# Kernel tuning notes

Hardware: AMD Instinct MI355X
Metric: run time of the kernel (lower is better)

The kernel has to match this reference:

```python
import jax, jax.numpy as jnp
import numpy as np

EMBED_DIM = 1024
NUM_HEAD = 16
HEAD_DIM = EMBED_DIM // NUM_HEAD
SCALE = HEAD_DIM ** -0.5
EPS = 1e-6


def setup_inputs() -> dict:
    key = jax.random.key(0)
    ks = jax.random.split(key, 8)
    B, N, K, D = 4, 2048, 2048, EMBED_DIM
    x = jax.random.normal(ks[0], (B, N, D), dtype=jnp.float32)
    ctx = jax.random.normal(ks[1], (B, K, D), dtype=jnp.float32)
    w_std = 0.02
    q_w = jax.random.normal(ks[2], (D, D), dtype=jnp.float32) * w_std  # [in, out]
    q_b = jnp.zeros((D,), dtype=jnp.float32)
    kv_w = jax.random.normal(ks[3], (D, 2 * D), dtype=jnp.float32) * w_std
    kv_b = jnp.zeros((2 * D,), dtype=jnp.float32)
    proj_w = jax.random.normal(ks[4], (D, D), dtype=jnp.float32) * w_std
    proj_b = jnp.zeros((D,), dtype=jnp.float32)
    return {"x": x, "ctx": ctx, "q_w": q_w, "q_b": q_b,
            "kv_w": kv_w, "kv_b": kv_b, "proj_w": proj_w, "proj_b": proj_b}


def rms_norm(t):
    return t * jax.lax.rsqrt(jnp.mean(t * t, axis=-1, keepdims=True) + EPS)


def reference(x, ctx, q_w, q_b, kv_w, kv_b, proj_w, proj_b):
    B, N, D = x.shape
    Kc = ctx.shape[1]
    H, Hd = NUM_HEAD, HEAD_DIM
    ctxn = rms_norm(ctx)
    q = (x @ q_w + q_b).reshape(B, N, H, Hd)                 # bnhd
    kv = (ctxn @ kv_w + kv_b).reshape(B, Kc, 2, H, Hd)
    k, v = kv[:, :, 0], kv[:, :, 1]                          # bkhd
    logits = jnp.einsum('bnhd,bkhd->bhnk', q * SCALE, k)
    logits = jnp.clip(logits, -10.0, 10.0)
    attn = jax.nn.softmax(logits, axis=-1)                   # bhnk
    out = jnp.einsum('bhnk,bkhd->bnhd', attn, v).reshape(B, N, D)
    out = out @ proj_w + proj_b
    return out, attn.mean()
```

## Files before the change

kernel.cpp:

```cpp
#include <hip/hip_runtime.h>
#include <hip/hip_bf16.h>
#include <stdint.h>


typedef __bf16 bf16_t;
typedef __bf16 bf16x8 __attribute__((ext_vector_type(8)));
typedef __bf16 bf16x4 __attribute__((ext_vector_type(4)));
typedef short  s16x4  __attribute__((ext_vector_type(4)));
typedef float  f32x4  __attribute__((ext_vector_type(4)));

#define BB 4
#define NN 2048
#define KC 2048
#define DD 1024
#define NH 16
#define HD 64
#define QSCALE 0.18033688011112042f
#define CLIP2  14.426950408889634f

__device__ __forceinline__ f32x4 mfma_16x16x32(bf16x8 a, bf16x8 b, f32x4 c) {
  return __builtin_amdgcn_mfma_f32_16x16x32_bf16(a, b, c, 0, 0, 0);
}
__device__ __forceinline__ f32x4 mfma_16x16x16(s16x4 a, s16x4 b, f32x4 c) {
  return __builtin_amdgcn_mfma_f32_16x16x16bf16_1k(a, b, c, 0, 0, 0);
}

__device__ __forceinline__ void gl_lds16(const bf16_t* g, bf16_t* l) {
  __builtin_amdgcn_global_load_lds(
      (const __attribute__((address_space(1))) void*)g,
      (__attribute__((address_space(3))) void*)l, 16, 0, 0);
}

__global__ __launch_bounds__(256) void cvt_f32_bf16(const float* __restrict__ in,
                                                    bf16_t* __restrict__ out, int n4) {
  int i = blockIdx.x * 256 + threadIdx.x;
  if (i >= n4) return;
  float4 v = ((const float4*)in)[i];
  bf16x4 o = {(bf16_t)v.x, (bf16_t)v.y, (bf16_t)v.z, (bf16_t)v.w};
  ((bf16x4*)out)[i] = o;
}

__global__ __launch_bounds__(256) void rmsnorm_rows(const float* __restrict__ in,
                                                    bf16_t* __restrict__ out) {
  int row = blockIdx.x, tid = threadIdx.x;
  float4 v = ((const float4*)(in + (size_t)row * DD))[tid];
  float ss = v.x * v.x + v.y * v.y + v.z * v.z + v.w * v.w;
#pragma unroll
  for (int m = 1; m < 64; m <<= 1) ss += __shfl_xor(ss, m);
  __shared__ float wsum[4];
  if ((tid & 63) == 0) wsum[tid >> 6] = ss;
  __syncthreads();
  float total = wsum[0] + wsum[1] + wsum[2] + wsum[3];
  float scale = rsqrtf(total * (1.0f / (float)DD) + 1e-6f);
  bf16x4 o = {(bf16_t)(v.x * scale), (bf16_t)(v.y * scale),
              (bf16_t)(v.z * scale), (bf16_t)(v.w * scale)};
  ((bf16x4*)(out + (size_t)row * DD))[tid] = o;
}

__global__ __launch_bounds__(256) void transpose_w(const float* __restrict__ W,
                                                   bf16_t* __restrict__ WT, int R, int C) {
  __shared__ float tile[32][33];
  int tx = threadIdx.x & 31, ty = threadIdx.x >> 5;
  int r0 = blockIdx.y * 32, c0 = blockIdx.x * 32;
#pragma unroll
  for (int i = 0; i < 4; i++) tile[ty + 8 * i][tx] = W[(size_t)(r0 + ty + 8 * i) * C + c0 + tx];
  __syncthreads();
#pragma unroll
  for (int i = 0; i < 4; i++)
    WT[(size_t)(c0 + ty + 8 * i) * R + r0 + tx] = (bf16_t)tile[tx][ty + 8 * i];
}

template <int OUT_F32>
__global__ __launch_bounds__(256, 2) void gemm_bt(const bf16_t* __restrict__ A,
                                                  const bf16_t* __restrict__ Bt,
                                                  const float* __restrict__ bias,
                                                  void* __restrict__ Cout, int M, int N,
                                                  int Kd, float alpha) {
  __shared__ bf16_t As[128 * 32];
  __shared__ bf16_t Bs[128 * 32];
  int tid = threadIdx.x;
  int w = tid >> 6, lane = tid & 63;
  int quad = lane >> 4, l16 = lane & 15;
  int row0 = blockIdx.y * 128, col0 = blockIdx.x * 128;
  int wm = (w >> 1) * 64, wn = (w & 1) * 64;

  f32x4 acc[4][4];
#pragma unroll
  for (int i = 0; i < 4; i++)
#pragma unroll
    for (int j = 0; j < 4; j++) acc[i][j] = (f32x4){0.f, 0.f, 0.f, 0.f};

  for (int kk = 0; kk < Kd; kk += 32) {
#pragma unroll
    for (int call = 0; call < 2; call++) {
      int c = w * 128 + call * 64 + lane;
      gl_lds16(&A[(size_t)(row0 + (c >> 2)) * Kd + kk + (c & 3) * 8],
               &As[(w * 128 + call * 64) * 8]);
      gl_lds16(&Bt[(size_t)(col0 + (c >> 2)) * Kd + kk + (c & 3) * 8],
               &Bs[(w * 128 + call * 64) * 8]);
    }
    __syncthreads();
    bf16x8 af[4], bfr[4];
#pragma unroll
    for (int mi = 0; mi < 4; mi++)
      af[mi] = *(const bf16x8*)&As[(wm + mi * 16 + l16) * 32 + quad * 8];
#pragma unroll
    for (int ni = 0; ni < 4; ni++)
      bfr[ni] = *(const bf16x8*)&Bs[(wn + ni * 16 + l16) * 32 + quad * 8];
#pragma unroll
    for (int mi = 0; mi < 4; mi++)
#pragma unroll
      for (int ni = 0; ni < 4; ni++) acc[mi][ni] = mfma_16x16x32(af[mi], bfr[ni], acc[mi][ni]);
    __syncthreads();
  }

#pragma unroll
  for (int ni = 0; ni < 4; ni++) {
    int col = col0 + wn + ni * 16 + l16;
    float bv = bias[col];
#pragma unroll
    for (int mi = 0; mi < 4; mi++) {
#pragma unroll
      for (int r = 0; r < 4; r++) {
        int row = row0 + wm + mi * 16 + quad * 4 + r;
        float v = (acc[mi][ni][r] + bv) * alpha;
        if (OUT_F32)
          ((float*)Cout)[(size_t)row * N + col] = v;
        else
          ((bf16_t*)Cout)[(size_t)row * N + col] = (bf16_t)v;
      }
    }
  }
}

__global__ __launch_bounds__(256) void transpose_v(const bf16_t* __restrict__ kvbuf,
                                                   bf16_t* __restrict__ vT) {
  __shared__ bf16_t tile[64][72];
  int bh = blockIdx.y;
  int b = bh >> 4, h = bh & 15;
  int kc0 = blockIdx.x * 64;
  int tid = threadIdx.x;
#pragma unroll
  for (int i = 0; i < 2; i++) {
    int ch = tid + i * 256;
    int key = ch >> 3, cc = ch & 7;
    *(bf16x8*)&tile[key][cc * 8] =
        *(const bf16x8*)&kvbuf[((size_t)b * KC + kc0 + key) * (2 * DD) + DD + h * HD + cc * 8];
  }
  __syncthreads();
#pragma unroll
  for (int i = 0; i < 2; i++) {
    int ch = tid + i * 256;
    int hd = ch >> 3, cc = ch & 7;
    bf16x8 v;
#pragma unroll
    for (int e = 0; e < 8; e++) v[e] = tile[cc * 8 + e][hd];
    *(bf16x8*)&vT[((size_t)bh * HD + hd) * KC + kc0 + cc * 8] = v;
  }
}

__global__ __launch_bounds__(256, 4) void flash_attn(const bf16_t* __restrict__ qbuf,
                                                     const bf16_t* __restrict__ kvbuf,
                                                     const bf16_t* __restrict__ vT,
                                                     bf16_t* __restrict__ attn_out) {
  __shared__ bf16_t Qs[128][72];
  __shared__ bf16_t Ks[64][72];
  __shared__ bf16_t Vs[64][72];
  __shared__ __align__(16) float rsh[4][32];
  int tid = threadIdx.x, w = tid >> 6, lane = tid & 63;
  int quad = lane >> 4, l16 = lane & 15;
  int bid = blockIdx.x;
  int xcd = bid & 7, slot = bid >> 3;
  int bh = xcd * 8 + (slot >> 4);
  int qt = slot & 15;
  int b = bh >> 4, h = bh & 15;
  int n0 = qt * 128;

#pragma unroll
  for (int i = 0; i < 4; i++) {
    int ch = tid + i * 256;
    int r = ch >> 3, cc = ch & 7;
    *(bf16x8*)&Qs[r][cc * 8] =
        *(const bf16x8*)&qbuf[((size_t)b * NN + n0 + r) * DD + h * HD + cc * 8];
  }
  __syncthreads();
  bf16x8 qf[2][2];
#pragma unroll
  for (int qi = 0; qi < 2; qi++)
#pragma unroll
    for (int dc = 0; dc < 2; dc++)
      qf[qi][dc] = *(const bf16x8*)&Qs[w * 32 + qi * 16 + l16][dc * 32 + quad * 8];

  f32x4 o[2][4];
  float rs[2] = {0.f, 0.f};
#pragma unroll
  for (int qi = 0; qi < 2; qi++)
#pragma unroll
    for (int hb = 0; hb < 4; hb++) o[qi][hb] = (f32x4){0.f, 0.f, 0.f, 0.f};

  const size_t kvbase = (size_t)b * KC * (2 * DD) + (size_t)h * HD;
  const size_t vtbase = (size_t)bh * HD * KC;

  for (int kc0 = 0; kc0 < KC; kc0 += 64) {
    __syncthreads();
#pragma unroll
    for (int i = 0; i < 2; i++) {
      int ch = tid + i * 256;
      int r = ch >> 3, cc = ch & 7;
      *(bf16x8*)&Ks[r][cc * 8] =
          *(const bf16x8*)&kvbuf[kvbase + (size_t)(kc0 + r) * (2 * DD) + cc * 8];
      *(bf16x8*)&Vs[r][cc * 8] = *(const bf16x8*)&vT[vtbase + (size_t)r * KC + kc0 + cc * 8];
    }
    __syncthreads();

#pragma unroll
    for (int ki = 0; ki < 4; ki++) {
      bf16x8 kf0 = *(const bf16x8*)&Ks[ki * 16 + l16][quad * 8];
      bf16x8 kf1 = *(const bf16x8*)&Ks[ki * 16 + l16][32 + quad * 8];
      s16x4 pf[2];
#pragma unroll
      for (int qi = 0; qi < 2; qi++) {
        f32x4 s = (f32x4){0.f, 0.f, 0.f, 0.f};
        s = mfma_16x16x32(kf0, qf[qi][0], s);
        s = mfma_16x16x32(kf1, qf[qi][1], s);
        bf16x4 pb;
#pragma unroll
        for (int r = 0; r < 4; r++) {
          float p = __builtin_amdgcn_exp2f(__builtin_amdgcn_fmed3f(s[r], -CLIP2, CLIP2));
          rs[qi] += p;
          pb[r] = (bf16_t)p;
        }
        pf[qi] = __builtin_bit_cast(s16x4, pb);
      }
#pragma unroll
      for (int hb = 0; hb < 4; hb++) {
        s16x4 vf = *(const s16x4*)&Vs[hb * 16 + l16][ki * 16 + quad * 4];
#pragma unroll
        for (int qi = 0; qi < 2; qi++) o[qi][hb] = mfma_16x16x16(pf[qi], vf, o[qi][hb]);
      }
    }
  }

#pragma unroll
  for (int qi = 0; qi < 2; qi++) {
    float v = rs[qi];
    v += __shfl_xor(v, 16);
    v += __shfl_xor(v, 32);
    rs[qi] = v;
  }
  if (quad == 0) {
    rsh[w][l16] = 1.0f / rs[0];
    rsh[w][16 + l16] = 1.0f / rs[1];
  }
  __syncthreads();

#pragma unroll
  for (int qi = 0; qi < 2; qi++) {
    f32x4 rv = *(const f32x4*)&rsh[w][qi * 16 + quad * 4];
#pragma unroll
    for (int hb = 0; hb < 4; hb++)
#pragma unroll
      for (int r = 0; r < 4; r++) {
        int row = n0 + w * 32 + qi * 16 + quad * 4 + r;
        int col = h * HD + hb * 16 + l16;
        attn_out[((size_t)b * NN + row) * DD + col] = (bf16_t)(o[qi][hb][r] * rv[r]);
      }
  }
}

__global__ void write_mean(float* out) { out[0] = 1.0f / 2048.0f; }

extern "C" void kernel_launch(void* const* d_in, const int* in_sizes, int n_in, void* d_out,
                              int out_size, void* d_ws, size_t ws_size, hipStream_t stream) {
  const float* x      = (const float*)d_in[0];
  const float* ctx    = (const float*)d_in[1];
  const float* q_w    = (const float*)d_in[2];
  const float* q_b    = (const float*)d_in[3];
  const float* kv_w   = (const float*)d_in[4];
  const float* kv_b   = (const float*)d_in[5];
  const float* proj_w = (const float*)d_in[6];
  const float* proj_b = (const float*)d_in[7];
  float* out = (float*)d_out;
  char* ws = (char*)d_ws;

  bf16_t* xb    = (bf16_t*)(ws + 0);
  bf16_t* ctxn  = (bf16_t*)(ws + 16777216);
  bf16_t* qwT   = (bf16_t*)(ws + 33554432);
  bf16_t* kvwT  = (bf16_t*)(ws + 35651584);
  bf16_t* pwT   = (bf16_t*)(ws + 39845888);
  bf16_t* qbuf  = (bf16_t*)(ws + 41943040);
  bf16_t* kvbuf = (bf16_t*)(ws + 58720256);
  bf16_t* vT       = ctxn;
  bf16_t* attn_out = xb;

  cvt_f32_bf16<<<8192, 256, 0, stream>>>(x, xb, (BB * NN * DD) / 4);
  rmsnorm_rows<<<BB * KC, 256, 0, stream>>>(ctx, ctxn);
  transpose_w<<<dim3(32, 32), 256, 0, stream>>>(q_w, qwT, DD, DD);
  transpose_w<<<dim3(64, 32), 256, 0, stream>>>(kv_w, kvwT, DD, 2 * DD);
  transpose_w<<<dim3(32, 32), 256, 0, stream>>>(proj_w, pwT, DD, DD);
  gemm_bt<0><<<dim3(8, 64), 256, 0, stream>>>(xb, qwT, q_b, qbuf, BB * NN, DD, DD, QSCALE);
  gemm_bt<0><<<dim3(16, 64), 256, 0, stream>>>(ctxn, kvwT, kv_b, kvbuf, BB * KC, 2 * DD, DD, 1.0f);
  transpose_v<<<dim3(KC / 64, BB * NH), 256, 0, stream>>>(kvbuf, vT);
  flash_attn<<<1024, 256, 0, stream>>>(qbuf, kvbuf, vT, attn_out);
  gemm_bt<1><<<dim3(8, 64), 256, 0, stream>>>(attn_out, pwT, proj_b, out, BB * NN, DD, DD, 1.0f);
  write_mean<<<1, 1, 0, stream>>>(out + (size_t)out_size - 1);
}
```

Before: 364.5 us.

## Split attention KV range across waves with register-direct loads and LDS reduction

The flash attention kernel now gives each block 64 query rows and has the four waves split the key range, each wave handling 32 keys per 128-key step. K and V fragments are loaded straight from global memory into registers instead of being staged through LDS. Partial outputs and row sums are then combined across waves through LDS, and the output is written with coalesced stores via an LDS staging tile. The PV product uses the wider 16x16x32 MFMA in place of 16x16x16. This removes the per-iteration barriers and LDS traffic, at the cost of more registers (occupancy hint drops from 4 to 3), uncoalesced direct global loads, and a final cross-wave reduction.

```diff
diff --git a/kernel.cpp b/kernel.cpp
--- a/kernel.cpp
+++ b/kernel.cpp
@@ -20,9 +20,6 @@
 
 __device__ __forceinline__ f32x4 mfma_16x16x32(bf16x8 a, bf16x8 b, f32x4 c) {
   return __builtin_amdgcn_mfma_f32_16x16x32_bf16(a, b, c, 0, 0, 0);
-}
-__device__ __forceinline__ f32x4 mfma_16x16x16(s16x4 a, s16x4 b, f32x4 c) {
-  return __builtin_amdgcn_mfma_f32_16x16x16bf16_1k(a, b, c, 0, 0, 0);
 }
 
 __device__ __forceinline__ void gl_lds16(const bf16_t* g, bf16_t* l) {
@@ -159,70 +156,73 @@
   }
 }
 
-__global__ __launch_bounds__(256, 4) void flash_attn(const bf16_t* __restrict__ qbuf,
+__global__ __launch_bounds__(256, 3) void flash_attn(const bf16_t* __restrict__ qbuf,
                                                      const bf16_t* __restrict__ kvbuf,
                                                      const bf16_t* __restrict__ vT,
                                                      bf16_t* __restrict__ attn_out) {
-  __shared__ bf16_t Qs[128][72];
-  __shared__ bf16_t Ks[64][72];
-  __shared__ bf16_t Vs[64][72];
-  __shared__ __align__(16) float rsh[4][32];
+  __shared__ float Obuf[2][64][68];
+  __shared__ float rsh[4][64];
+  __shared__ float rsinv[64];
+  __shared__ bf16_t outS[64][72];
+
   int tid = threadIdx.x, w = tid >> 6, lane = tid & 63;
   int quad = lane >> 4, l16 = lane & 15;
   int bid = blockIdx.x;
   int xcd = bid & 7, slot = bid >> 3;
-  int bh = xcd * 8 + (slot >> 4);
-  int qt = slot & 15;
+  int bh = xcd * 8 + (slot >> 5);
+  int qt = slot & 31;
   int b = bh >> 4, h = bh & 15;
-  int n0 = qt * 128;
-
-#pragma unroll
-  for (int i = 0; i < 4; i++) {
-    int ch = tid + i * 256;
-    int r = ch >> 3, cc = ch & 7;
-    *(bf16x8*)&Qs[r][cc * 8] =
-        *(const bf16x8*)&qbuf[((size_t)b * NN + n0 + r) * DD + h * HD + cc * 8];
-  }
-  __syncthreads();
-  bf16x8 qf[2][2];
-#pragma unroll
-  for (int qi = 0; qi < 2; qi++)
-#pragma unroll
-    for (int dc = 0; dc < 2; dc++)
-      qf[qi][dc] = *(const bf16x8*)&Qs[w * 32 + qi * 16 + l16][dc * 32 + quad * 8];
-
-  f32x4 o[2][4];
-  float rs[2] = {0.f, 0.f};
-#pragma unroll
-  for (int qi = 0; qi < 2; qi++)
-#pragma unroll
-    for (int hb = 0; hb < 4; hb++) o[qi][hb] = (f32x4){0.f, 0.f, 0.f, 0.f};
+  int n0 = qt * 64;
 
   const size_t kvbase = (size_t)b * KC * (2 * DD) + (size_t)h * HD;
   const size_t vtbase = (size_t)bh * HD * KC;
 
-  for (int kc0 = 0; kc0 < KC; kc0 += 64) {
-    __syncthreads();
-#pragma unroll
-    for (int i = 0; i < 2; i++) {
-      int ch = tid + i * 256;
-      int r = ch >> 3, cc = ch & 7;
-      *(bf16x8*)&Ks[r][cc * 8] =
-          *(const bf16x8*)&kvbuf[kvbase + (size_t)(kc0 + r) * (2 * DD) + cc * 8];
-      *(bf16x8*)&Vs[r][cc * 8] = *(const bf16x8*)&vT[vtbase + (size_t)r * KC + kc0 + cc * 8];
-    }
-    __syncthreads();
-
-#pragma unroll
-    for (int ki = 0; ki < 4; ki++) {
-      bf16x8 kf0 = *(const bf16x8*)&Ks[ki * 16 + l16][quad * 8];
-      bf16x8 kf1 = *(const bf16x8*)&Ks[ki * 16 + l16][32 + quad * 8];
-      s16x4 pf[2];
-#pragma unroll
-      for (int qi = 0; qi < 2; qi++) {
+  bf16x8 qf[4][2];
+#pragma unroll
+  for (int qi = 0; qi < 4; qi++)
+#pragma unroll
+    for (int dc = 0; dc < 2; dc++)
+      qf[qi][dc] = *(const bf16x8*)&qbuf[((size_t)b * NN + n0 + qi * 16 + l16) * DD + h * HD +
+                                         dc * 32 + quad * 8];
+
+  f32x4 o[4][4];
+#pragma unroll
+  for (int qi = 0; qi < 4; qi++)
+#pragma unroll
+    for (int hb = 0; hb < 4; hb++) o[qi][hb] = (f32x4){0.f, 0.f, 0.f, 0.f};
+  float rs[4] = {0.f, 0.f, 0.f, 0.f};
+
+  for (int kc0 = 0; kc0 < KC; kc0 += 128) {
+    int wk = kc0 + w * 32;
+    bf16x8 kf[2][2];
+#pragma unroll
+    for (int g = 0; g < 2; g++)
+#pragma unroll
+      for (int dc = 0; dc < 2; dc++)
+        kf[g][dc] = *(const bf16x8*)&kvbuf[kvbase + (size_t)(wk + g * 16 + l16) * (2 * DD) +
+                                           dc * 32 + quad * 8];
+    union {
+      bf16x8 v8;
+      s16x4 h[2];
+    } vB[4];
+#pragma unroll
+    for (int hb = 0; hb < 4; hb++) {
+      const bf16_t* vrow = &vT[vtbase + (size_t)(hb * 16 + l16) * KC + wk + quad * 4];
+      vB[hb].h[0] = *(const s16x4*)(vrow);
+      vB[hb].h[1] = *(const s16x4*)(vrow + 16);
+    }
+
+#pragma unroll
+    for (int qi = 0; qi < 4; qi++) {
+      union {
+        bf16x8 v8;
+        bf16x4 h[2];
+      } pf;
+#pragma unroll
+      for (int g = 0; g < 2; g++) {
         f32x4 s = (f32x4){0.f, 0.f, 0.f, 0.f};
-        s = mfma_16x16x32(kf0, qf[qi][0], s);
-        s = mfma_16x16x32(kf1, qf[qi][1], s);
+        s = mfma_16x16x32(kf[g][0], qf[qi][0], s);
+        s = mfma_16x16x32(kf[g][1], qf[qi][1], s);
         bf16x4 pb;
 #pragma unroll
         for (int r = 0; r < 4; r++) {
@@ -230,41 +230,65 @@
           rs[qi] += p;
           pb[r] = (bf16_t)p;
         }
-        pf[qi] = __builtin_bit_cast(s16x4, pb);
+        pf.h[g] = pb;
       }
 #pragma unroll
-      for (int hb = 0; hb < 4; hb++) {
-        s16x4 vf = *(const s16x4*)&Vs[hb * 16 + l16][ki * 16 + quad * 4];
-#pragma unroll
-        for (int qi = 0; qi < 2; qi++) o[qi][hb] = mfma_16x16x16(pf[qi], vf, o[qi][hb]);
-      }
-    }
-  }
-
-#pragma unroll
-  for (int qi = 0; qi < 2; qi++) {
+      for (int hb = 0; hb < 4; hb++) o[qi][hb] = mfma_16x16x32(pf.v8, vB[hb].v8, o[qi][hb]);
+    }
+  }
+
+#pragma unroll
+  for (int qi = 0; qi < 4; qi++) {
     float v = rs[qi];
     v += __shfl_xor(v, 16);
     v += __shfl_xor(v, 32);
-    rs[qi] = v;
-  }
-  if (quad == 0) {
-    rsh[w][l16] = 1.0f / rs[0];
-    rsh[w][16 + l16] = 1.0f / rs[1];
-  }
-  __syncthreads();
-
-#pragma unroll
-  for (int qi = 0; qi < 2; qi++) {
-    f32x4 rv = *(const f32x4*)&rsh[w][qi * 16 + quad * 4];
-#pragma unroll
-    for (int hb = 0; hb < 4; hb++)
-#pragma unroll
-      for (int r = 0; r < 4; r++) {
-        int row = n0 + w * 32 + qi * 16 + quad * 4 + r;
-        int col = h * HD + hb * 16 + l16;
-        attn_out[((size_t)b * NN + row) * DD + col] = (bf16_t)(o[qi][hb][r] * rv[r]);
+    if (quad == 0) rsh[w][qi * 16 + l16] = v;
+  }
+  if (w >= 2) {
+#pragma unroll
+    for (int qi = 0; qi < 4; qi++)
+#pragma unroll
+      for (int hb = 0; hb < 4; hb++)
+        *(f32x4*)&Obuf[w - 2][hb * 16 + l16][qi * 16 + quad * 4] = o[qi][hb];
+  }
+  __syncthreads();
+  if (w < 2) {
+#pragma unroll
+    for (int qi = 0; qi < 4; qi++)
+#pragma unroll
+      for (int hb = 0; hb < 4; hb++)
+        o[qi][hb] += *(const f32x4*)&Obuf[w][hb * 16 + l16][qi * 16 + quad * 4];
+  }
+  if (w == 2) rsinv[lane] = 1.0f / (rsh[0][lane] + rsh[1][lane] + rsh[2][lane] + rsh[3][lane]);
+  __syncthreads();
+  if (w == 1) {
+#pragma unroll
+    for (int qi = 0; qi < 4; qi++)
+#pragma unroll
+      for (int hb = 0; hb < 4; hb++)
+        *(f32x4*)&Obuf[0][hb * 16 + l16][qi * 16 + quad * 4] = o[qi][hb];
+  }
+  __syncthreads();
+  if (w == 0) {
+#pragma unroll
+    for (int qi = 0; qi < 4; qi++) {
+      f32x4 ri = *(const f32x4*)&rsinv[qi * 16 + quad * 4];
+#pragma unroll
+      for (int hb = 0; hb < 4; hb++) {
+        f32x4 ov = o[qi][hb] + *(const f32x4*)&Obuf[0][hb * 16 + l16][qi * 16 + quad * 4];
+#pragma unroll
+        for (int r = 0; r < 4; r++)
+          outS[qi * 16 + quad * 4 + r][hb * 16 + l16] = (bf16_t)(ov[r] * ri[r]);
       }
+    }
+  }
+  __syncthreads();
+#pragma unroll
+  for (int i = 0; i < 2; i++) {
+    int idx = tid + i * 256;
+    int row = idx >> 3, c = idx & 7;
+    *(bf16x8*)&attn_out[((size_t)b * NN + n0 + row) * DD + h * HD + c * 8] =
+        *(const bf16x8*)&outS[row][c * 8];
   }
 }
 
@@ -301,7 +325,7 @@
   gemm_bt<0><<<dim3(8, 64), 256, 0, stream>>>(xb, qwT, q_b, qbuf, BB * NN, DD, DD, QSCALE);
   gemm_bt<0><<<dim3(16, 64), 256, 0, stream>>>(ctxn, kvwT, kv_b, kvbuf, BB * KC, 2 * DD, DD, 1.0f);
   transpose_v<<<dim3(KC / 64, BB * NH), 256, 0, stream>>>(kvbuf, vT);
-  flash_attn<<<1024, 256, 0, stream>>>(qbuf, kvbuf, vT, attn_out);
+  flash_attn<<<2048, 256, 0, stream>>>(qbuf, kvbuf, vT, attn_out);
   gemm_bt<1><<<dim3(8, 64), 256, 0, stream>>>(attn_out, pwT, proj_b, out, BB * NN, DD, DD, 1.0f);
   write_mean<<<1, 1, 0, stream>>>(out + (size_t)out_size - 1);
 }
```

After: 431.9 us. +18.5%, slower.
